# Optimization experiments

Measured on AMD Instinct MI355X. Metric: run time of the kernel, lower is better.

## Reference

```python
import jax, jax.numpy as jnp
import numpy as np

B, S, D_MODEL, HEAD, D_KV = 8, 1024, 1024, 16, 64


def setup_inputs() -> dict:
    key = jax.random.key(0)
    ks = jax.random.split(key, 10)
    std = 1.0 / np.sqrt(D_MODEL)
    inp = {
        "queries": jax.random.normal(ks[0], (B, S, D_MODEL), jnp.float32),
        "keys": jax.random.normal(ks[1], (B, S, D_MODEL), jnp.float32),
        "values": jax.random.normal(ks[2], (B, S, D_MODEL), jnp.float32),
        "group_prob": jax.random.uniform(ks[3], (B, 1, S, S), jnp.float32),
        "attention_mask": jax.random.randint(ks[4], (B, 1, S, S), 0, 2, jnp.int32),
        "Wq": jax.random.normal(ks[5], (HEAD * D_KV, D_MODEL), jnp.float32) * std,
        "bq": jnp.zeros((HEAD * D_KV,), jnp.float32),
        "Wk": jax.random.normal(ks[6], (HEAD * D_KV, D_MODEL), jnp.float32) * std,
        "bk": jnp.zeros((HEAD * D_KV,), jnp.float32),
        "Wv": jax.random.normal(ks[7], (HEAD * D_KV, D_MODEL), jnp.float32) * std,
        "bv": jnp.zeros((HEAD * D_KV,), jnp.float32),
    }
    return inp


def reference(queries, keys, values, group_prob, attention_mask, Wq, bq, Wk, bk, Wv, bv):
    b, nq = queries.shape[:2]
    # QKV projections -> [b, head, seq, d_kv]
    q = (queries @ Wq.T + bq).reshape(b, nq, HEAD, D_KV).transpose(0, 2, 1, 3)
    k = (keys @ Wk.T + bk).reshape(b, -1, HEAD, D_KV).transpose(0, 2, 1, 3)
    v = (values @ Wv.T + bv).reshape(b, -1, HEAD, D_KV).transpose(0, 2, 1, 3)
    # scaled scores [b, head, nq, nk]
    att = jnp.einsum("bhqd,bhkd->bhqk", q, k) / np.sqrt(D_KV).astype(np.float32)
    # NOTE: the original torch code calls att.masked_fill(...) (out-of-place)
    # and discards the result, so attention_mask has no effect. Replicated here.
    att = jax.nn.softmax(att, axis=-1)
    att = att * group_prob  # post-softmax group scaling (breaks fused SDPA)
    out = jnp.einsum("bhqk,bhkd->bhqd", att, v)
    return out.transpose(0, 2, 1, 3).reshape(b, nq, HEAD * D_KV)
```

## Files before the change

### kernel.cpp

```cpp
#include <hip/hip_runtime.h>

#define B_SZ 8
#define S_SZ 1024
#define DM   1024
#define NH   16
#define DK   64

typedef __bf16 bf16;
typedef __bf16 bf16x8 __attribute__((ext_vector_type(8)));
typedef float  f32x4  __attribute__((ext_vector_type(4)));

__device__ __forceinline__ f32x4 mfma16x16x32(bf16x8 a, bf16x8 b, f32x4 c) {
    return __builtin_amdgcn_mfma_f32_16x16x32_bf16(a, b, c, 0, 0, 0);
}

__global__ __launch_bounds__(256, 2)
void qkv_proj_kernel(const float* __restrict__ Xq, const float* __restrict__ Xk,
                     const float* __restrict__ Xv,
                     const float* __restrict__ Wq, const float* __restrict__ Wk,
                     const float* __restrict__ Wv,
                     const float* __restrict__ bq, const float* __restrict__ bk,
                     const float* __restrict__ bv,
                     bf16* __restrict__ qb, bf16* __restrict__ kb,
                     bf16* __restrict__ vb)
{
    const int z = blockIdx.z;
    const float* X    = (z == 0) ? Xq : (z == 1) ? Xk : Xv;
    const float* W    = (z == 0) ? Wq : (z == 1) ? Wk : Wv;
    const float* bias = (z == 0) ? bq : (z == 1) ? bk : bv;

    __shared__ bf16 Ash[128][40];
    __shared__ bf16 Bsh[128][40];

    const int tid  = threadIdx.x;
    const int wid  = tid >> 6;
    const int lane = tid & 63;
    const int quad = lane >> 4;
    const int l16  = lane & 15;
    const int wm   = wid >> 1, wn = wid & 1;
    const int bm   = blockIdx.x, bn = blockIdx.y;

    f32x4 acc[4][4] = {};

    for (int k0 = 0; k0 < DM; k0 += 32) {
        #pragma unroll
        for (int i = 0; i < 4; ++i) {
            const int e   = (i * 256 + tid) * 4;
            const int row = e >> 5;
            const int col = e & 31;
            const float4 av  = *(const float4*)(X + (size_t)(bm * 128 + row) * DM + k0 + col);
            const float4 bv4 = *(const float4*)(W + (size_t)(bn * 128 + row) * DM + k0 + col);
            union { bf16 h[4]; uint2 u; } pa, pb;
            pa.h[0] = (bf16)av.x;  pa.h[1] = (bf16)av.y;
            pa.h[2] = (bf16)av.z;  pa.h[3] = (bf16)av.w;
            pb.h[0] = (bf16)bv4.x; pb.h[1] = (bf16)bv4.y;
            pb.h[2] = (bf16)bv4.z; pb.h[3] = (bf16)bv4.w;
            *(uint2*)&Ash[row][col] = pa.u;
            *(uint2*)&Bsh[row][col] = pb.u;
        }
        __syncthreads();
        bf16x8 af[4], bfr[4];
        #pragma unroll
        for (int mi = 0; mi < 4; ++mi)
            af[mi] = *(const bf16x8*)&Ash[wm * 64 + mi * 16 + l16][quad * 8];
        #pragma unroll
        for (int ni = 0; ni < 4; ++ni)
            bfr[ni] = *(const bf16x8*)&Bsh[wn * 64 + ni * 16 + l16][quad * 8];
        #pragma unroll
        for (int mi = 0; mi < 4; ++mi)
            #pragma unroll
            for (int ni = 0; ni < 4; ++ni)
                acc[mi][ni] = mfma16x16x32(af[mi], bfr[ni], acc[mi][ni]);
        __syncthreads();
    }

    #pragma unroll
    for (int ni = 0; ni < 4; ++ni) {
        const int n   = bn * 128 + wn * 64 + ni * 16 + l16;
        const float bv_ = bias[n];
        const int h = n >> 6, d = n & 63;
        #pragma unroll
        for (int mi = 0; mi < 4; ++mi) {
            const int m0 = bm * 128 + wm * 64 + mi * 16 + quad * 4;
            const int b  = m0 >> 10;
            const int s0 = m0 & 1023;
            if (z == 2) {
                union { bf16 h4[4]; uint2 u; } pk;
                #pragma unroll
                for (int r = 0; r < 4; ++r) pk.h4[r] = (bf16)(acc[mi][ni][r] + bv_);
                *(uint2*)(vb + ((size_t)((b * NH + h) * DK + d)) * S_SZ + s0) = pk.u;
            } else {
                bf16* dst      = (z == 0) ? qb : kb;
                const float sc = (z == 0) ? 0.125f : 1.0f;
                #pragma unroll
                for (int r = 0; r < 4; ++r)
                    dst[((size_t)(b * NH + h) * S_SZ + (s0 + r)) * DK + d] =
                        (bf16)((acc[mi][ni][r] + bv_) * sc);
            }
        }
    }
}

__global__ __launch_bounds__(256, 2)
void attn_kernel(const bf16* __restrict__ qb, const bf16* __restrict__ kb,
                 const bf16* __restrict__ vb, const float* __restrict__ gp,
                 float* __restrict__ out)
{
    __shared__ bf16 Ksh[64][72];
    __shared__ bf16 Vsh[64][72];
    __shared__ bf16 Psh[4][16][72];

    const int tid  = threadIdx.x;
    const int wid  = tid >> 6;
    const int lane = tid & 63;
    const int quad = lane >> 4;
    const int l16  = lane & 15;

    const int bh = blockIdx.x;
    const int qt = blockIdx.y;
    const int b  = bh >> 4;
    const int h  = bh & (NH - 1);

    const bf16* qrow = qb + ((size_t)bh * S_SZ + qt * 64 + wid * 16 + l16) * DK;
    const bf16x8 qf0 = *(const bf16x8*)(qrow + quad * 8);
    const bf16x8 qf1 = *(const bf16x8*)(qrow + 32 + quad * 8);

    f32x4 acc_o[4] = {};
    float m_r[4], l_r[4];
    #pragma unroll
    for (int r = 0; r < 4; ++r) { m_r[r] = -1e30f; l_r[r] = 0.0f; }

    const int qrow0 = qt * 64 + wid * 16 + quad * 4;
    const float* gpb = gp + ((size_t)b * S_SZ + qrow0) * S_SZ;

    for (int kt = 0; kt < S_SZ / 64; ++kt) {
        __syncthreads();
        #pragma unroll
        for (int i = 0; i < 2; ++i) {
            const int e   = (i * 256 + tid) * 8;
            const int row = e >> 6;
            const int col = e & 63;
            *(bf16x8*)&Ksh[row][col] =
                *(const bf16x8*)(kb + ((size_t)bh * S_SZ + kt * 64 + row) * DK + col);
            *(bf16x8*)&Vsh[row][col] =
                *(const bf16x8*)(vb + ((size_t)bh * DK + row) * S_SZ + kt * 64 + col);
        }
        float gpv[4][4];
        #pragma unroll
        for (int nb = 0; nb < 4; ++nb)
            #pragma unroll
            for (int r = 0; r < 4; ++r)
                gpv[nb][r] = gpb[(size_t)r * S_SZ + kt * 64 + nb * 16 + l16];
        __syncthreads();

        f32x4 sc[4] = {};
        #pragma unroll
        for (int nb = 0; nb < 4; ++nb) {
            const bf16x8 kf0 = *(const bf16x8*)&Ksh[nb * 16 + l16][quad * 8];
            const bf16x8 kf1 = *(const bf16x8*)&Ksh[nb * 16 + l16][32 + quad * 8];
            sc[nb] = mfma16x16x32(qf0, kf0, sc[nb]);
            sc[nb] = mfma16x16x32(qf1, kf1, sc[nb]);
        }

        float tmax[4];
        #pragma unroll
        for (int r = 0; r < 4; ++r)
            tmax[r] = fmaxf(fmaxf(sc[0][r], sc[1][r]), fmaxf(sc[2][r], sc[3][r]));
        #pragma unroll
        for (int off = 1; off < 16; off <<= 1)
            #pragma unroll
            for (int r = 0; r < 4; ++r)
                tmax[r] = fmaxf(tmax[r], __shfl_xor(tmax[r], off, 64));

        float alpha[4], p[4][4], tsum[4];
        #pragma unroll
        for (int r = 0; r < 4; ++r) {
            const float mn = fmaxf(m_r[r], tmax[r]);
            alpha[r] = __expf(m_r[r] - mn);
            m_r[r]   = mn;
            tsum[r]  = 0.0f;
        }
        #pragma unroll
        for (int nb = 0; nb < 4; ++nb)
            #pragma unroll
            for (int r = 0; r < 4; ++r) {
                p[nb][r] = __expf(sc[nb][r] - m_r[r]);
                tsum[r] += p[nb][r];
            }
        #pragma unroll
        for (int off = 1; off < 16; off <<= 1)
            #pragma unroll
            for (int r = 0; r < 4; ++r)
                tsum[r] += __shfl_xor(tsum[r], off, 64);
        #pragma unroll
        for (int r = 0; r < 4; ++r)
            l_r[r] = l_r[r] * alpha[r] + tsum[r];
        #pragma unroll
        for (int ni = 0; ni < 4; ++ni)
            #pragma unroll
            for (int r = 0; r < 4; ++r)
                acc_o[ni][r] *= alpha[r];

        #pragma unroll
        for (int nb = 0; nb < 4; ++nb)
            #pragma unroll
            for (int r = 0; r < 4; ++r)
                Psh[wid][quad * 4 + r][nb * 16 + l16] = (bf16)(p[nb][r] * gpv[nb][r]);

        const bf16x8 pf0 = *(const bf16x8*)&Psh[wid][l16][quad * 8];
        const bf16x8 pf1 = *(const bf16x8*)&Psh[wid][l16][32 + quad * 8];
        #pragma unroll
        for (int ni = 0; ni < 4; ++ni) {
            const bf16x8 vf0 = *(const bf16x8*)&Vsh[ni * 16 + l16][quad * 8];
            const bf16x8 vf1 = *(const bf16x8*)&Vsh[ni * 16 + l16][32 + quad * 8];
            acc_o[ni] = mfma16x16x32(pf0, vf0, acc_o[ni]);
            acc_o[ni] = mfma16x16x32(pf1, vf1, acc_o[ni]);
        }
    }

    #pragma unroll
    for (int r = 0; r < 4; ++r) {
        const float inv = 1.0f / l_r[r];
        float* orow = out + ((size_t)b * S_SZ + qrow0 + r) * DM + h * DK;
        #pragma unroll
        for (int ni = 0; ni < 4; ++ni)
            orow[ni * 16 + l16] = acc_o[ni][r] * inv;
    }
}

extern "C" void kernel_launch(void* const* d_in, const int* in_sizes, int n_in,
                              void* d_out, int out_size, void* d_ws, size_t ws_size,
                              hipStream_t stream) {
    const float* queries = (const float*)d_in[0];
    const float* keys    = (const float*)d_in[1];
    const float* values  = (const float*)d_in[2];
    const float* gp      = (const float*)d_in[3];
    const float* Wq = (const float*)d_in[5];
    const float* bq = (const float*)d_in[6];
    const float* Wk = (const float*)d_in[7];
    const float* bk = (const float*)d_in[8];
    const float* Wv = (const float*)d_in[9];
    const float* bv = (const float*)d_in[10];
    float* out = (float*)d_out;

    bf16* qb = (bf16*)d_ws;
    bf16* kb = qb + (size_t)B_SZ * NH * S_SZ * DK;
    bf16* vb = kb + (size_t)B_SZ * NH * S_SZ * DK;
    (void)ws_size; (void)in_sizes; (void)n_in; (void)out_size;

    dim3 g1(DM * B_SZ / 128 , DM / 128 , 3);
    qkv_proj_kernel<<<g1, 256, 0, stream>>>(queries, keys, values,
                                            Wq, Wk, Wv, bq, bk, bv, qb, kb, vb);
    dim3 g2(B_SZ * NH , S_SZ / 64 , 1);
    attn_kernel<<<g2, 256, 0, stream>>>(qb, kb, vb, gp, out);
}
```

Before: 400.4 us.

## Pre-convert inputs to bf16, use async LDS loads, enlarge attention query tile

Adds a separate kernel that converts the X and W fp32 inputs to bf16 in workspace. The projection GEMM then loads bf16 tiles with global_load_lds direct-to-LDS copies over a 64-wide K step. The attention kernel uses the same async copies for K/V and processes 32 query rows per wave (128 per block), which halves K/V reloads. The risks are the extra pass over the fp32 inputs, bank conflicts from the unpadded LDS layouts, and higher register pressure in the attention kernel.

After: 399.6 us. Within noise of the previous version (-0.2%).

```diff
diff --git a/kernel.cpp b/kernel.cpp
--- a/kernel.cpp
+++ b/kernel.cpp
@@ -14,23 +14,56 @@
     return __builtin_amdgcn_mfma_f32_16x16x32_bf16(a, b, c, 0, 0, 0);
 }
 
+typedef const __attribute__((address_space(1))) void* gptr_t;
+typedef __attribute__((address_space(3))) void*       sptr_t;
+__device__ __forceinline__ void async_cp16(const void* g, void* s) {
+    __builtin_amdgcn_global_load_lds((gptr_t)g, (sptr_t)s, 16, 0, 0);
+}
+
+__global__ __launch_bounds__(256)
+void cvt_kernel(const float* __restrict__ x0, const float* __restrict__ x1,
+                const float* __restrict__ x2, const float* __restrict__ w0,
+                const float* __restrict__ w1, const float* __restrict__ w2,
+                bf16* __restrict__ xb, bf16* __restrict__ wb)
+{
+    const int z = blockIdx.y;
+    const float* src;
+    bf16* dst;
+    int n;
+    if (z < 3) {
+        src = (z == 0) ? x0 : (z == 1) ? x1 : x2;
+        dst = xb + (size_t)z * (8u * 1024 * 1024);
+        n = 8 * 1024 * 1024;
+    } else {
+        const int w = z - 3;
+        src = (w == 0) ? w0 : (w == 1) ? w1 : w2;
+        dst = wb + (size_t)w * (1024 * 1024);
+        n = 1024 * 1024;
+    }
+    const int idx = (blockIdx.x * 256 + threadIdx.x) * 8;
+    if (idx >= n) return;
+    const float4 a = *(const float4*)(src + idx);
+    const float4 c = *(const float4*)(src + idx + 4);
+    union { bf16 h[8]; uint4 u; } pk;
+    pk.h[0] = (bf16)a.x; pk.h[1] = (bf16)a.y; pk.h[2] = (bf16)a.z; pk.h[3] = (bf16)a.w;
+    pk.h[4] = (bf16)c.x; pk.h[5] = (bf16)c.y; pk.h[6] = (bf16)c.z; pk.h[7] = (bf16)c.w;
+    *(uint4*)(dst + idx) = pk.u;
+}
+
 __global__ __launch_bounds__(256, 2)
-void qkv_proj_kernel(const float* __restrict__ Xq, const float* __restrict__ Xk,
-                     const float* __restrict__ Xv,
-                     const float* __restrict__ Wq, const float* __restrict__ Wk,
-                     const float* __restrict__ Wv,
-                     const float* __restrict__ bq, const float* __restrict__ bk,
-                     const float* __restrict__ bv,
-                     bf16* __restrict__ qb, bf16* __restrict__ kb,
-                     bf16* __restrict__ vb)
+void qkv_gemm(const bf16* __restrict__ xb, const bf16* __restrict__ wb,
+              const float* __restrict__ bq, const float* __restrict__ bk,
+              const float* __restrict__ bv,
+              bf16* __restrict__ qb, bf16* __restrict__ kb,
+              bf16* __restrict__ vb)
 {
     const int z = blockIdx.z;
-    const float* X    = (z == 0) ? Xq : (z == 1) ? Xk : Xv;
-    const float* W    = (z == 0) ? Wq : (z == 1) ? Wk : Wv;
+    const bf16* A = xb + (size_t)z * (8u * 1024 * 1024);
+    const bf16* Bm = wb + (size_t)z * (1024 * 1024);
     const float* bias = (z == 0) ? bq : (z == 1) ? bk : bv;
 
-    __shared__ bf16 Ash[128][40];
-    __shared__ bf16 Bsh[128][40];
+    __shared__ bf16 Ash[128 * 64];
+    __shared__ bf16 Bsh[128 * 64];
 
     const int tid  = threadIdx.x;
     const int wid  = tid >> 6;
@@ -42,41 +75,38 @@
 
     f32x4 acc[4][4] = {};
 
-    for (int k0 = 0; k0 < DM; k0 += 32) {
+    for (int k0 = 0; k0 < DM; k0 += 64) {
+        __syncthreads();
         #pragma unroll
         for (int i = 0; i < 4; ++i) {
-            const int e   = (i * 256 + tid) * 4;
-            const int row = e >> 5;
-            const int col = e & 31;
-            const float4 av  = *(const float4*)(X + (size_t)(bm * 128 + row) * DM + k0 + col);
-            const float4 bv4 = *(const float4*)(W + (size_t)(bn * 128 + row) * DM + k0 + col);
-            union { bf16 h[4]; uint2 u; } pa, pb;
-            pa.h[0] = (bf16)av.x;  pa.h[1] = (bf16)av.y;
-            pa.h[2] = (bf16)av.z;  pa.h[3] = (bf16)av.w;
-            pb.h[0] = (bf16)bv4.x; pb.h[1] = (bf16)bv4.y;
-            pb.h[2] = (bf16)bv4.z; pb.h[3] = (bf16)bv4.w;
-            *(uint2*)&Ash[row][col] = pa.u;
-            *(uint2*)&Bsh[row][col] = pb.u;
+            const int e   = (i * 256 + tid) * 8;
+            const int row = e >> 6;
+            const int col = e & 63;
+            async_cp16(A + (size_t)(bm * 128 + row) * DM + k0 + col, &Ash[e]);
+            async_cp16(Bm + (size_t)(bn * 128 + row) * DM + k0 + col, &Bsh[e]);
         }
         __syncthreads();
-        bf16x8 af[4], bfr[4];
-        #pragma unroll
-        for (int mi = 0; mi < 4; ++mi)
-            af[mi] = *(const bf16x8*)&Ash[wm * 64 + mi * 16 + l16][quad * 8];
-        #pragma unroll
-        for (int ni = 0; ni < 4; ++ni)
-            bfr[ni] = *(const bf16x8*)&Bsh[wn * 64 + ni * 16 + l16][quad * 8];
-        #pragma unroll
-        for (int mi = 0; mi < 4; ++mi)
+
+        #pragma unroll
+        for (int ks = 0; ks < 2; ++ks) {
+            bf16x8 af[4], bfr[4];
+            #pragma unroll
+            for (int mi = 0; mi < 4; ++mi)
+                af[mi] = *(const bf16x8*)&Ash[(wm * 64 + mi * 16 + l16) * 64 + ks * 32 + quad * 8];
             #pragma unroll
             for (int ni = 0; ni < 4; ++ni)
-                acc[mi][ni] = mfma16x16x32(af[mi], bfr[ni], acc[mi][ni]);
-        __syncthreads();
+                bfr[ni] = *(const bf16x8*)&Bsh[(wn * 64 + ni * 16 + l16) * 64 + ks * 32 + quad * 8];
+            #pragma unroll
+            for (int mi = 0; mi < 4; ++mi)
+                #pragma unroll
+                for (int ni = 0; ni < 4; ++ni)
+                    acc[mi][ni] = mfma16x16x32(af[mi], bfr[ni], acc[mi][ni]);
+        }
     }
 
     #pragma unroll
     for (int ni = 0; ni < 4; ++ni) {
-        const int n   = bn * 128 + wn * 64 + ni * 16 + l16;
+        const int n    = bn * 128 + wn * 64 + ni * 16 + l16;
         const float bv_ = bias[n];
         const int h = n >> 6, d = n & 63;
         #pragma unroll
@@ -106,9 +136,9 @@
                  const bf16* __restrict__ vb, const float* __restrict__ gp,
                  float* __restrict__ out)
 {
-    __shared__ bf16 Ksh[64][72];
-    __shared__ bf16 Vsh[64][72];
-    __shared__ bf16 Psh[4][16][72];
+    __shared__ bf16 Ksh[64 * 64];
+    __shared__ bf16 Vsh[64 * 64];
+    __shared__ bf16 Psh[4][32][72];
 
     const int tid  = threadIdx.x;
     const int wid  = tid >> 6;
@@ -121,17 +151,27 @@
     const int b  = bh >> 4;
     const int h  = bh & (NH - 1);
 
-    const bf16* qrow = qb + ((size_t)bh * S_SZ + qt * 64 + wid * 16 + l16) * DK;
-    const bf16x8 qf0 = *(const bf16x8*)(qrow + quad * 8);
-    const bf16x8 qf1 = *(const bf16x8*)(qrow + 32 + quad * 8);
-
-    f32x4 acc_o[4] = {};
-    float m_r[4], l_r[4];
-    #pragma unroll
-    for (int r = 0; r < 4; ++r) { m_r[r] = -1e30f; l_r[r] = 0.0f; }
-
-    const int qrow0 = qt * 64 + wid * 16 + quad * 4;
-    const float* gpb = gp + ((size_t)b * S_SZ + qrow0) * S_SZ;
+    const int q0 = qt * 128 + wid * 32;
+
+    bf16x8 qf[2][2];
+    #pragma unroll
+    for (int mi = 0; mi < 2; ++mi) {
+        const bf16* qr = qb + ((size_t)bh * S_SZ + q0 + mi * 16 + l16) * DK;
+        qf[mi][0] = *(const bf16x8*)(qr + quad * 8);
+        qf[mi][1] = *(const bf16x8*)(qr + 32 + quad * 8);
+    }
+
+    f32x4 acc_o[2][4] = {};
+    float m_r[2][4], l_r[2][4];
+    #pragma unroll
+    for (int mi = 0; mi < 2; ++mi)
+        #pragma unroll
+        for (int r = 0; r < 4; ++r) { m_r[mi][r] = -1e30f; l_r[mi][r] = 0.0f; }
+
+    const float* gpq[2];
+    #pragma unroll
+    for (int mi = 0; mi < 2; ++mi)
+        gpq[mi] = gp + ((size_t)b * S_SZ + q0 + mi * 16 + quad * 4) * S_SZ;
 
     for (int kt = 0; kt < S_SZ / 64; ++kt) {
         __syncthreads();
@@ -140,92 +180,109 @@
             const int e   = (i * 256 + tid) * 8;
             const int row = e >> 6;
             const int col = e & 63;
-            *(bf16x8*)&Ksh[row][col] =
-                *(const bf16x8*)(kb + ((size_t)bh * S_SZ + kt * 64 + row) * DK + col);
-            *(bf16x8*)&Vsh[row][col] =
-                *(const bf16x8*)(vb + ((size_t)bh * DK + row) * S_SZ + kt * 64 + col);
-        }
-        float gpv[4][4];
-        #pragma unroll
-        for (int nb = 0; nb < 4; ++nb)
+            async_cp16(kb + (size_t)bh * (S_SZ * DK) + kt * 4096 + e, &Ksh[e]);
+            async_cp16(vb + ((size_t)bh * DK + row) * S_SZ + kt * 64 + col, &Vsh[e]);
+        }
+        float gpv[2][4][4];
+        #pragma unroll
+        for (int mi = 0; mi < 2; ++mi)
+            #pragma unroll
+            for (int nb = 0; nb < 4; ++nb)
+                #pragma unroll
+                for (int r = 0; r < 4; ++r)
+                    gpv[mi][nb][r] = gpq[mi][(size_t)r * S_SZ + kt * 64 + nb * 16 + l16];
+        __syncthreads();
+
+        f32x4 sc[2][4] = {};
+        #pragma unroll
+        for (int nb = 0; nb < 4; ++nb) {
+            const bf16x8 kf0 = *(const bf16x8*)&Ksh[(nb * 16 + l16) * 64 + quad * 8];
+            const bf16x8 kf1 = *(const bf16x8*)&Ksh[(nb * 16 + l16) * 64 + 32 + quad * 8];
+            #pragma unroll
+            for (int mi = 0; mi < 2; ++mi) {
+                sc[mi][nb] = mfma16x16x32(qf[mi][0], kf0, sc[mi][nb]);
+                sc[mi][nb] = mfma16x16x32(qf[mi][1], kf1, sc[mi][nb]);
+            }
+        }
+
+        #pragma unroll
+        for (int mi = 0; mi < 2; ++mi) {
+            float tmax[4];
             #pragma unroll
             for (int r = 0; r < 4; ++r)
-                gpv[nb][r] = gpb[(size_t)r * S_SZ + kt * 64 + nb * 16 + l16];
-        __syncthreads();
-
-        f32x4 sc[4] = {};
-        #pragma unroll
-        for (int nb = 0; nb < 4; ++nb) {
-            const bf16x8 kf0 = *(const bf16x8*)&Ksh[nb * 16 + l16][quad * 8];
-            const bf16x8 kf1 = *(const bf16x8*)&Ksh[nb * 16 + l16][32 + quad * 8];
-            sc[nb] = mfma16x16x32(qf0, kf0, sc[nb]);
-            sc[nb] = mfma16x16x32(qf1, kf1, sc[nb]);
-        }
-
-        float tmax[4];
-        #pragma unroll
-        for (int r = 0; r < 4; ++r)
-            tmax[r] = fmaxf(fmaxf(sc[0][r], sc[1][r]), fmaxf(sc[2][r], sc[3][r]));
-        #pragma unroll
-        for (int off = 1; off < 16; off <<= 1)
+                tmax[r] = fmaxf(fmaxf(sc[mi][0][r], sc[mi][1][r]),
+                                fmaxf(sc[mi][2][r], sc[mi][3][r]));
+            #pragma unroll
+            for (int off = 1; off < 16; off <<= 1)
+                #pragma unroll
+                for (int r = 0; r < 4; ++r)
+                    tmax[r] = fmaxf(tmax[r], __shfl_xor(tmax[r], off, 64));
+
+            float alpha[4], p[4][4], tsum[4];
+            #pragma unroll
+            for (int r = 0; r < 4; ++r) {
+                const float mn = fmaxf(m_r[mi][r], tmax[r]);
+                alpha[r] = __expf(m_r[mi][r] - mn);
+                m_r[mi][r] = mn;
+                tsum[r] = 0.0f;
+            }
+            #pragma unroll
+            for (int nb = 0; nb < 4; ++nb)
+                #pragma unroll
+                for (int r = 0; r < 4; ++r) {
+                    p[nb][r] = __expf(sc[mi][nb][r] - m_r[mi][r]);
+                    tsum[r] += p[nb][r];
+                }
+            #pragma unroll
+            for (int off = 1; off < 16; off <<= 1)
+                #pragma unroll
+                for (int r = 0; r < 4; ++r)
+                    tsum[r] += __shfl_xor(tsum[r], off, 64);
             #pragma unroll
             for (int r = 0; r < 4; ++r)
-                tmax[r] = fmaxf(tmax[r], __shfl_xor(tmax[r], off, 64));
-
-        float alpha[4], p[4][4], tsum[4];
+                l_r[mi][r] = l_r[mi][r] * alpha[r] + tsum[r];
+            #pragma unroll
+            for (int ni = 0; ni < 4; ++ni)
+                #pragma unroll
+                for (int r = 0; r < 4; ++r)
+                    acc_o[mi][ni][r] *= alpha[r];
+
+            #pragma unroll
+            for (int nb = 0; nb < 4; ++nb)
+                #pragma unroll
+                for (int r = 0; r < 4; ++r)
+                    Psh[wid][mi * 16 + quad * 4 + r][nb * 16 + l16] =
+                        (bf16)(p[nb][r] * gpv[mi][nb][r]);
+        }
+
+        bf16x8 pf[2][2];
+        #pragma unroll
+        for (int mi = 0; mi < 2; ++mi) {
+            pf[mi][0] = *(const bf16x8*)&Psh[wid][mi * 16 + l16][quad * 8];
+            pf[mi][1] = *(const bf16x8*)&Psh[wid][mi * 16 + l16][32 + quad * 8];
+        }
+        #pragma unroll
+        for (int ni = 0; ni < 4; ++ni) {
+            const bf16x8 vf0 = *(const bf16x8*)&Vsh[(ni * 16 + l16) * 64 + quad * 8];
+            const bf16x8 vf1 = *(const bf16x8*)&Vsh[(ni * 16 + l16) * 64 + 32 + quad * 8];
+            #pragma unroll
+            for (int mi = 0; mi < 2; ++mi) {
+                acc_o[mi][ni] = mfma16x16x32(pf[mi][0], vf0, acc_o[mi][ni]);
+                acc_o[mi][ni] = mfma16x16x32(pf[mi][1], vf1, acc_o[mi][ni]);
+            }
+        }
+    }
+
+    #pragma unroll
+    for (int mi = 0; mi < 2; ++mi)
         #pragma unroll
         for (int r = 0; r < 4; ++r) {
-            const float mn = fmaxf(m_r[r], tmax[r]);
-            alpha[r] = __expf(m_r[r] - mn);
-            m_r[r]   = mn;
-            tsum[r]  = 0.0f;
-        }
-        #pragma unroll
-        for (int nb = 0; nb < 4; ++nb)
-            #pragma unroll
-            for (int r = 0; r < 4; ++r) {
-                p[nb][r] = __expf(sc[nb][r] - m_r[r]);
-                tsum[r] += p[nb][r];
-            }
-        #pragma unroll
-        for (int off = 1; off < 16; off <<= 1)
-            #pragma unroll
-            for (int r = 0; r < 4; ++r)
-                tsum[r] += __shfl_xor(tsum[r], off, 64);
-        #pragma unroll
-        for (int r = 0; r < 4; ++r)
-            l_r[r] = l_r[r] * alpha[r] + tsum[r];
-        #pragma unroll
-        for (int ni = 0; ni < 4; ++ni)
-            #pragma unroll
-            for (int r = 0; r < 4; ++r)
-                acc_o[ni][r] *= alpha[r];
-
-        #pragma unroll
-        for (int nb = 0; nb < 4; ++nb)
-            #pragma unroll
-            for (int r = 0; r < 4; ++r)
-                Psh[wid][quad * 4 + r][nb * 16 + l16] = (bf16)(p[nb][r] * gpv[nb][r]);
-
-        const bf16x8 pf0 = *(const bf16x8*)&Psh[wid][l16][quad * 8];
-        const bf16x8 pf1 = *(const bf16x8*)&Psh[wid][l16][32 + quad * 8];
-        #pragma unroll
-        for (int ni = 0; ni < 4; ++ni) {
-            const bf16x8 vf0 = *(const bf16x8*)&Vsh[ni * 16 + l16][quad * 8];
-            const bf16x8 vf1 = *(const bf16x8*)&Vsh[ni * 16 + l16][32 + quad * 8];
-            acc_o[ni] = mfma16x16x32(pf0, vf0, acc_o[ni]);
-            acc_o[ni] = mfma16x16x32(pf1, vf1, acc_o[ni]);
-        }
-    }
-
-    #pragma unroll
-    for (int r = 0; r < 4; ++r) {
-        const float inv = 1.0f / l_r[r];
-        float* orow = out + ((size_t)b * S_SZ + qrow0 + r) * DM + h * DK;
-        #pragma unroll
-        for (int ni = 0; ni < 4; ++ni)
-            orow[ni * 16 + l16] = acc_o[ni][r] * inv;
-    }
+            const float inv = 1.0f / l_r[mi][r];
+            float* orow = out + ((size_t)b * S_SZ + q0 + mi * 16 + quad * 4 + r) * DM + h * DK;
+            #pragma unroll
+            for (int ni = 0; ni < 4; ++ni)
+                orow[ni * 16 + l16] = acc_o[mi][ni][r] * inv;
+        }
 }
 
 extern "C" void kernel_launch(void* const* d_in, const int* in_sizes, int n_in,
@@ -243,14 +300,19 @@
     const float* bv = (const float*)d_in[10];
     float* out = (float*)d_out;
 
-    bf16* qb = (bf16*)d_ws;
+    bf16* xb = (bf16*)d_ws;
+    bf16* wb = xb + (size_t)3 * 8 * 1024 * 1024;
+    bf16* qb = wb + (size_t)3 * 1024 * 1024;
     bf16* kb = qb + (size_t)B_SZ * NH * S_SZ * DK;
     bf16* vb = kb + (size_t)B_SZ * NH * S_SZ * DK;
     (void)ws_size; (void)in_sizes; (void)n_in; (void)out_size;
 
-    dim3 g1(DM * B_SZ / 128 , DM / 128 , 3);
-    qkv_proj_kernel<<<g1, 256, 0, stream>>>(queries, keys, values,
-                                            Wq, Wk, Wv, bq, bk, bv, qb, kb, vb);
-    dim3 g2(B_SZ * NH , S_SZ / 64 , 1);
+    dim3 gc(4096, 6);
+    cvt_kernel<<<gc, 256, 0, stream>>>(queries, keys, values, Wq, Wk, Wv, xb, wb);
+
+    dim3 g1(64, 8, 3);
+    qkv_gemm<<<g1, 256, 0, stream>>>(xb, wb, bq, bk, bv, qb, kb, vb);
+
+    dim3 g2(B_SZ * NH , S_SZ / 128 , 1);
     attn_kernel<<<g2, 256, 0, stream>>>(qb, kb, vb, gp, out);
 }
```
